# Optimization experiments

Hardware: AMD Instinct MI355X
Metric: run time of the kernel (lower is better)

The kernel has to match this reference:

```python
import jax, jax.numpy as jnp
import numpy as np

D_MODEL = 1024
D_FF = 4096
N_HEADS = 16
HEAD_DIM = D_MODEL // N_HEADS
EPS = 1e-6
B, S = 4, 2048


def _linear_params(key, d_in, d_out):
    kw, kb = jax.random.split(key)
    scale = 1.0 / np.sqrt(d_in)
    w = jax.random.uniform(kw, (d_in, d_out), minval=-scale, maxval=scale, dtype=jnp.float32)
    b = jax.random.uniform(kb, (d_out,), minval=-scale, maxval=scale, dtype=jnp.float32)
    return w, b


def setup_inputs() -> dict:
    key = jax.random.key(0)
    ks = jax.random.split(key, 16)
    x = jax.random.normal(ks[0], (B, S, D_MODEL), dtype=jnp.float32)
    enc = jax.random.normal(ks[1], (B, S, D_MODEL), dtype=jnp.float32)
    # masked self-attention params
    wq1, bq1 = _linear_params(ks[2], D_MODEL, D_MODEL)
    wk1, bk1 = _linear_params(ks[3], D_MODEL, D_MODEL)
    wv1, bv1 = _linear_params(ks[4], D_MODEL, D_MODEL)
    wo1, bo1 = _linear_params(ks[5], D_MODEL, D_MODEL)
    # cross-attention params
    wq2, bq2 = _linear_params(ks[6], D_MODEL, D_MODEL)
    wk2, bk2 = _linear_params(ks[7], D_MODEL, D_MODEL)
    wv2, bv2 = _linear_params(ks[8], D_MODEL, D_MODEL)
    wo2, bo2 = _linear_params(ks[9], D_MODEL, D_MODEL)
    # feed-forward params
    wf1, bf1 = _linear_params(ks[10], D_MODEL, D_FF)
    wf2, bf2 = _linear_params(ks[11], D_FF, D_MODEL)
    # layer norms
    g1 = jnp.ones((D_MODEL,), jnp.float32); be1 = jnp.zeros((D_MODEL,), jnp.float32)
    g2 = jnp.ones((D_MODEL,), jnp.float32); be2 = jnp.zeros((D_MODEL,), jnp.float32)
    g3 = jnp.ones((D_MODEL,), jnp.float32); be3 = jnp.zeros((D_MODEL,), jnp.float32)
    return dict(x=x, encoder_output=enc,
                wq1=wq1, bq1=bq1, wk1=wk1, bk1=bk1, wv1=wv1, bv1=bv1, wo1=wo1, bo1=bo1,
                wq2=wq2, bq2=bq2, wk2=wk2, bk2=bk2, wv2=wv2, bv2=bv2, wo2=wo2, bo2=bo2,
                wf1=wf1, bf1=bf1, wf2=wf2, bf2=bf2,
                g1=g1, be1=be1, g2=g2, be2=be2, g3=g3, be3=be3)


def _layer_norm(x, g, b):
    mu = jnp.mean(x, axis=-1, keepdims=True)
    var = jnp.mean(jnp.square(x - mu), axis=-1, keepdims=True)
    return (x - mu) * jax.lax.rsqrt(var + EPS) * g + b


def _mha(q_in, k_in, v_in, wq, bq, wk, bk, wv, bv, wo, bo, causal):
    b, s, _ = q_in.shape
    q = (q_in @ wq + bq).reshape(b, s, N_HEADS, HEAD_DIM)
    k = (k_in @ wk + bk).reshape(b, -1, N_HEADS, HEAD_DIM)
    v = (v_in @ wv + bv).reshape(b, -1, N_HEADS, HEAD_DIM)
    scores = jnp.einsum('bqhd,bkhd->bhqk', q, k) / np.sqrt(HEAD_DIM)
    if causal:
        mask = jnp.tril(jnp.ones((s, s), dtype=bool))
        scores = jnp.where(mask, scores, jnp.finfo(scores.dtype).min)
    attn = jax.nn.softmax(scores, axis=-1)
    out = jnp.einsum('bhqk,bkhd->bqhd', attn, v).reshape(b, s, D_MODEL)
    return out @ wo + bo


def reference(x, encoder_output,
              wq1, bq1, wk1, bk1, wv1, bv1, wo1, bo1,
              wq2, bq2, wk2, bk2, wv2, bv2, wo2, bo2,
              wf1, bf1, wf2, bf2,
              g1, be1, g2, be2, g3, be3):
    # masked self-attention + residual + LN
    residual = x
    x = _mha(x, x, x, wq1, bq1, wk1, bk1, wv1, bv1, wo1, bo1, causal=True)
    x = _layer_norm(x + residual, g1, be1)
    # cross-attention (note: q=enc, k=enc, v=x as in the original) + residual + LN
    residual = x
    x = _mha(encoder_output, encoder_output, x, wq2, bq2, wk2, bk2, wv2, bv2, wo2, bo2, causal=False)
    x = _layer_norm(x + residual, g2, be2)
    # feed-forward (dropout=0 -> identity in eval) + residual + LN
    residual = x
    x = jax.nn.relu(x @ wf1 + bf1) @ wf2 + bf2
    x = _layer_norm(x + residual, g3, be3)
    return x
```

## Files before the change

kernel.cpp:

```cpp
#include <hip/hip_runtime.h>


typedef _Float16 f16;
typedef _Float16 f16x8 __attribute__((ext_vector_type(8)));
typedef _Float16 f16x4 __attribute__((ext_vector_type(4)));
typedef __fp16 fp16x2 __attribute__((ext_vector_type(2)));
typedef float f32x4 __attribute__((ext_vector_type(4)));
typedef float f32x16 __attribute__((ext_vector_type(16)));
typedef unsigned int u32;

#define AS1 __attribute__((address_space(1)))
#define AS3 __attribute__((address_space(3)))

constexpr int S_LEN = 2048;
constexpr int DM    = 1024;

constexpr long OFF_W   = 0;
constexpr long OFF_XB  = 32L  << 20;
constexpr long OFF_ENC = 48L  << 20;
constexpr long OFF_Q   = 64L  << 20;
constexpr long OFF_K   = 80L  << 20;
constexpr long OFF_V   = 96L  << 20;
constexpr long OFF_VT  = 112L << 20;
constexpr long OFF_AC  = 128L << 20;
constexpr long OFF_HID = 144L << 20;
constexpr long OFF_F1  = 208L << 20;
constexpr long OFF_F2  = 240L << 20;
constexpr long OFF_F3  = 272L << 20;
constexpr long BUF_BYTES = 304L << 20;

__device__ alignas(4096) unsigned char g_buf[BUF_BYTES];

constexpr long WQ1T = OFF_W + (0L  << 20);
constexpr long WF1T = OFF_W + (16L << 20);
constexpr long WF2T = OFF_W + (24L << 20);
constexpr long WO1T = OFF_W + (6L  << 20);
constexpr long WQ2T = OFF_W + (8L  << 20);
constexpr long WV2T = OFF_W + (12L << 20);
constexpr long WO2T = OFF_W + (14L << 20);

__global__ __launch_bounds__(256) void cvt2_k(const float* __restrict__ x,
                                              const float* __restrict__ enc)
{
    const int bid = blockIdx.x;
    const bool second = bid >= 8192;
    const float* in = second ? enc : x;
    f16* out = (f16*)(g_buf + (second ? OFF_ENC : OFF_XB));
    long i = (long)(second ? bid - 8192 : bid) * 256 + threadIdx.x;
    float4 v = ((const float4*)in)[i];
    f16x4 h;
    h.x = (f16)v.x; h.y = (f16)v.y; h.z = (f16)v.z; h.w = (f16)v.w;
    *(f16x4*)(out + i * 4) = h;
}

struct TWJobs { const float* src[10]; };

__global__ __launch_bounds__(256) void transw_all_k(TWJobs jobs)
{
    __shared__ float t[32][33];
    const int bid = blockIdx.x;
    int j, local;
    if (bid < 8192)       { j = bid >> 10; local = bid & 1023; }
    else if (bid < 12288) { j = 8; local = bid - 8192; }
    else                  { j = 9; local = bid - 12288; }
    const int K = (j == 9) ? 4096 : 1024;
    const int N = (j == 8) ? 4096 : 1024;
    const int tnx = N >> 5;
    const int tx32 = local % tnx, ty32 = local / tnx;
    const long dstOff = (j < 8) ? (long)j * (2L << 20) : ((j == 8) ? WF1T : WF2T);
    const float* W = jobs.src[j];
    f16* Wt = (f16*)(g_buf + dstOff);

    int tx = threadIdx.x, ty = threadIdx.y;
    int c0 = tx32 * 32, r0 = ty32 * 32;
#pragma unroll
    for (int i = 0; i < 4; ++i)
        t[ty + 8*i][tx] = W[(long)(r0 + ty + 8*i) * N + c0 + tx];
    __syncthreads();
#pragma unroll
    for (int i = 0; i < 4; ++i)
        Wt[(long)(c0 + ty + 8*i) * K + r0 + tx] = (f16)t[tx][ty + 8*i];
}

template<int MODE>
__global__ __launch_bounds__(256) void gemm3_k(
    long aOff, long bOff, long cOff, long vtOff,
    const float* __restrict__ b0, const float* __restrict__ b1,
    const float* __restrict__ b2, const float* __restrict__ b3,
    int K, int lda, int ldb, int ldc, long chunkStride, int tvch)
{
    __shared__ alignas(16) f16 As[3][128 * 32];
    __shared__ alignas(16) f16 Bs[3][128 * 32];

    const int tid  = threadIdx.x;
    const int lane = tid & 63;
    const int w    = tid >> 6;
    const int cB   = lane & 15;
    const int hi   = lane >> 4;

    const int nwg = gridDim.x * gridDim.y;
    const int id  = blockIdx.y * gridDim.x + blockIdx.x;
    const int swz = (id & 7) * (nwg >> 3) + (id >> 3);
    const int bx  = swz % gridDim.x, by = swz / gridDim.x;
    const int row0 = by * 128, col0 = bx * 128;

    const f16* Ab = (const f16*)(g_buf + aOff);
    const f16* Bb = (const f16*)(g_buf + bOff);

    const int wr = (w >> 1) * 64;
    const int wc = (w & 1) * 64;

    f32x4 acc[4][4] = {};

    auto stage = [&](int buf, int kt) {
        const int kB = kt * 32;
        const int base = w * 64;
#pragma unroll
        for (int r = 0; r < 2; ++r) {
            const int idx  = r * 256 + base + lane;
            const int srow = idx >> 2, sb = idx & 3;
            const int gk = (sb ^ ((srow >> 1) & 3)) << 3;
            __builtin_amdgcn_global_load_lds(
                (const AS1 void*)(Ab + (long)(row0 + srow) * lda + kB + gk),
                (AS3 void*)(&As[buf][(r * 256 + base) * 8]), 16, 0, 0);
            __builtin_amdgcn_global_load_lds(
                (const AS1 void*)(Bb + (long)(col0 + srow) * ldb + kB + gk),
                (AS3 void*)(&Bs[buf][(r * 256 + base) * 8]), 16, 0, 0);
        }
    };

    const int nt = K >> 5;
    stage(0, 0);
    stage(1, 1);

    for (int t = 0; t < nt; ++t) {
        if (nt - t >= 2) asm volatile("s_waitcnt vmcnt(4)" ::: "memory");
        else             asm volatile("s_waitcnt vmcnt(0)" ::: "memory");
        __builtin_amdgcn_s_barrier();
        __builtin_amdgcn_sched_barrier(0);
        if (t + 2 < nt) stage((t + 2) % 3, t + 2);

        const int cur = t % 3;
        f16x8 af[4], bf[4];
#pragma unroll
        for (int m = 0; m < 4; ++m) {
            const int row = wr + m * 16 + cB;
            af[m] = *(const f16x8*)&As[cur][row * 32 + ((hi ^ ((row >> 1) & 3)) << 3)];
        }
#pragma unroll
        for (int n = 0; n < 4; ++n) {
            const int row = wc + n * 16 + cB;
            bf[n] = *(const f16x8*)&Bs[cur][row * 32 + ((hi ^ ((row >> 1) & 3)) << 3)];
        }
#pragma unroll
        for (int m = 0; m < 4; ++m)
#pragma unroll
            for (int n = 0; n < 4; ++n)
                acc[m][n] = __builtin_amdgcn_mfma_f32_16x16x32_f16(af[m], bf[n], acc[m][n], 0, 0, 0);
    }

    const int ch = col0 >> 10;
    const float* bp = (ch == 0) ? b0 : (ch == 1) ? b1 : (ch == 2) ? b2 : b3;

    if (MODE == 0 && ch == tvch) {
        f16* Vt = (f16*)(g_buf + vtOff);
#pragma unroll
        for (int m = 0; m < 4; ++m) {
#pragma unroll
            for (int n = 0; n < 4; ++n) {
                const int c = col0 + wc + n * 16 + cB;
                const int hh = (c >> 6) & 15, dd = c & 63;
                const float bv = bp[c & 1023];
                const int r0e = row0 + wr + m * 16 + hi * 4;
                const int bb = r0e >> 11, sS = r0e & 2047;
                f16x4 hv;
#pragma unroll
                for (int jj = 0; jj < 4; ++jj) hv[jj] = (f16)(acc[m][n][jj] + bv);
                *(f16x4*)(Vt + (((long)(bb * 16 + hh) * 64 + dd) * 2048 + sS)) = hv;
            }
        }
        return;
    }

    float* Cf = (float*)(g_buf + cOff);
    f16*  Ch = (f16*)(g_buf + cOff);
    const long cBase = (long)ch * chunkStride;
#pragma unroll
    for (int m = 0; m < 4; ++m) {
#pragma unroll
        for (int n = 0; n < 4; ++n) {
            const int c = col0 + wc + n * 16 + cB;
            const float bv = bp[c & 1023];
#pragma unroll
            for (int jj = 0; jj < 4; ++jj) {
                const int r = row0 + wr + m * 16 + hi * 4 + jj;
                float v = acc[m][n][jj] + bv;
                if constexpr (MODE == 1) v = fmaxf(v, 0.f);
                const long idx = cBase + (long)r * ldc + (c & 1023);
                if constexpr (MODE == 2) Cf[idx] = v;
                else                     Ch[idx] = (f16)v;
            }
        }
    }
}

template<int CAUSAL>
__global__ __launch_bounds__(256, 4) void flash_k(long qOff, long kOff, long vtOff, long oOff)
{
    __shared__ alignas(16) f16 KV[2][2][4096];

    const int tid  = threadIdx.x;
    const int lane = tid & 63;
    const int w    = tid >> 6;
    const int ql   = lane & 31;
    const int s    = lane >> 5;

    const int raw   = (int)blockIdx.y * (int)gridDim.x + (int)blockIdx.x;
    const int newid = (raw & 7) * 128 + (raw >> 3);
    const int bh    = newid >> 4;
    int qt = newid & 15;
    if (CAUSAL) qt = 15 - qt;

    const int b = bh >> 4, h = bh & 15;
    const int q0 = qt * 128;
    const long tokB = (long)b * S_LEN;

    const f16* Qb  = (const f16*)(g_buf + qOff);
    const f16* Kb  = (const f16*)(g_buf + kOff);
    const f16* Vtb = (const f16*)(g_buf + vtOff) + (long)bh * 64 * S_LEN;
    f16* Ob = (f16*)(g_buf + oOff);

    const int r8 = lane >> 3;
    const int c8 = lane & 7;
    const int sb = c8 ^ r8;
    const int nch = CAUSAL ? 2 * (qt + 1) : (S_LEN / 64);

    auto stage = [&](int buf, int c) {
        const int kv0s = c * 64;
#pragma unroll
        for (int t = 0; t < 2; ++t) {
            const int grp = w * 2 + t;
            const int row = grp * 8 + r8;
            __builtin_amdgcn_global_load_lds(
                (const AS1 void*)(Kb + (tokB + kv0s + row) * DM + h * 64 + sb * 8),
                (AS3 void*)(&KV[buf][0][grp * 512]), 16, 0, 0);
            __builtin_amdgcn_global_load_lds(
                (const AS1 void*)(Vtb + (long)row * S_LEN + kv0s + sb * 8),
                (AS3 void*)(&KV[buf][1][grp * 512]), 16, 0, 0);
        }
    };

    stage(0, 0);

    f16x8 qf[4];
    {
        const f16 hs = (f16)(0.125f * 1.44269504088896f);
        const f16* qrow = Qb + (tokB + q0 + w * 32 + ql) * DM + h * 64 + s * 8;
#pragma unroll
        for (int kk = 0; kk < 4; ++kk) {
            qf[kk] = *(const f16x8*)(qrow + kk * 16);
#pragma unroll
            for (int i = 0; i < 8; ++i) qf[kk][i] = qf[kk][i] * hs;
        }
    }

    f32x16 oacc[2] = {};
    float mrow = -1e30f, lrow = 0.f;

    for (int c = 0; c < nch; ++c) {
        const int cur = c & 1;
        const int kv0 = c * 64;

        asm volatile("s_waitcnt vmcnt(0) lgkmcnt(0)" ::: "memory");
        __builtin_amdgcn_sched_barrier(0);
        __builtin_amdgcn_s_barrier();
        __builtin_amdgcn_sched_barrier(0);
        if (c + 1 < nch) stage(cur ^ 1, c + 1);

        const bool active = !CAUSAL || (kv0 <= q0 + w * 32 + 31);
        if (active) {
            f32x16 p[2] = {};
#pragma unroll
            for (int kk = 0; kk < 4; ++kk) {
                const int t16 = (kk * 2 + s) ^ (ql & 7);
                f16x8 kf0 = *(const f16x8*)((const char*)&KV[cur][0][0] + ql * 128 + t16 * 16);
                f16x8 kf1 = *(const f16x8*)((const char*)&KV[cur][0][0] + (32 + ql) * 128 + t16 * 16);
                p[0] = __builtin_amdgcn_mfma_f32_32x32x16_f16(kf0, qf[kk], p[0], 0, 0, 0);
                p[1] = __builtin_amdgcn_mfma_f32_32x32x16_f16(kf1, qf[kk], p[1], 0, 0, 0);
            }

            if (CAUSAL && (kv0 + 63 > q0 + w * 32)) {
                const int q = q0 + w * 32 + ql;
#pragma unroll
                for (int v = 0; v < 2; ++v)
#pragma unroll
                    for (int r = 0; r < 16; ++r) {
                        const int kv = kv0 + v * 32 + (r & 3) + 8 * (r >> 2) + 4 * s;
                        if (kv > q) p[v][r] = -1e30f;
                    }
            }

            float rmax = fmaxf(p[0][0], p[0][1]);
#pragma unroll
            for (int r = 2; r < 16; r += 2) rmax = fmaxf(fmaxf(p[0][r], p[0][r + 1]), rmax);
#pragma unroll
            for (int r = 0; r < 16; r += 2) rmax = fmaxf(fmaxf(p[1][r], p[1][r + 1]), rmax);
            rmax = fmaxf(rmax, __shfl_xor(rmax, 32));

            if (!__all(rmax <= mrow + 8.0f)) {
                const float mn = fmaxf(mrow, rmax);
                const float alpha = __builtin_amdgcn_exp2f(mrow - mn);
                lrow *= alpha;
                mrow = mn;
#pragma unroll
                for (int r = 0; r < 16; ++r) {
                    const int qr = (r & 3) + 8 * (r >> 2) + 4 * s;
                    const float ab = __shfl(alpha, qr);
                    oacc[0][r] *= ab;
                    oacc[1][r] *= ab;
                }
            }

            u32 pk[2][4][2];
            float rsum = 0.f;
#pragma unroll
            for (int v = 0; v < 2; ++v)
#pragma unroll
                for (int a = 0; a < 4; ++a)
#pragma unroll
                    for (int cc = 0; cc < 2; ++cc) {
                        const float e0 = __builtin_amdgcn_exp2f(p[v][4 * a + 2 * cc] - mrow);
                        const float e1 = __builtin_amdgcn_exp2f(p[v][4 * a + 2 * cc + 1] - mrow);
                        rsum += e0 + e1;
                        union { fp16x2 h; u32 u; } cv;
                        cv.h = __builtin_amdgcn_cvt_pkrtz(e0, e1);
                        pk[v][a][cc] = cv.u;
                    }
            rsum += __shfl_xor(rsum, 32);
            lrow += rsum;

            u32 loc[2][2][2], exv[2][2][2];
#pragma unroll
            for (int v = 0; v < 2; ++v)
#pragma unroll
                for (int k1 = 0; k1 < 2; ++k1)
#pragma unroll
                    for (int cc = 0; cc < 2; ++cc) {
                        const u32 pe = pk[v][2 * k1][cc];
                        const u32 po = pk[v][2 * k1 + 1][cc];
                        loc[v][k1][cc] = s ? po : pe;
                        const u32 snd = s ? pe : po;
                        exv[v][k1][cc] = (u32)__shfl_xor((int)snd, 32);
                    }

#pragma unroll
            for (int ks = 0; ks < 4; ++ks) {
                const int v = ks >> 1, k1 = ks & 1;
                union { u32 u[4]; f16x8 hv; } pa;
                pa.u[0] = s ? exv[v][k1][0] : loc[v][k1][0];
                pa.u[1] = s ? exv[v][k1][1] : loc[v][k1][1];
                pa.u[2] = s ? loc[v][k1][0] : exv[v][k1][0];
                pa.u[3] = s ? loc[v][k1][1] : exv[v][k1][1];
                const int tv = (ks * 2 + s) ^ (ql & 7);
                f16x8 vf0 = *(const f16x8*)((const char*)&KV[cur][1][0] + ql * 128 + tv * 16);
                f16x8 vf1 = *(const f16x8*)((const char*)&KV[cur][1][0] + (32 + ql) * 128 + tv * 16);
                oacc[0] = __builtin_amdgcn_mfma_f32_32x32x16_f16(pa.hv, vf0, oacc[0], 0, 0, 0);
                oacc[1] = __builtin_amdgcn_mfma_f32_32x32x16_f16(pa.hv, vf1, oacc[1], 0, 0, 0);
            }
        }
    }

    asm volatile("s_waitcnt lgkmcnt(0)" ::: "memory");
    __builtin_amdgcn_sched_barrier(0);
    __builtin_amdgcn_s_barrier();

    f16* Es = ((f16*)&KV[0][0][0]) + w * 2304;
    const float linv = 1.0f / lrow;
#pragma unroll
    for (int r = 0; r < 16; ++r) {
        const int qr = (r & 3) + 8 * (r >> 2) + 4 * s;
        const float lb = __shfl(linv, qr);
        Es[qr * 72 + ql]      = (f16)(oacc[0][r] * lb);
        Es[qr * 72 + 32 + ql] = (f16)(oacc[1][r] * lb);
    }
    const int orow = lane >> 1;
    const int oh   = (lane & 1) * 32;
    const f16* srcp = ((const f16*)&KV[0][0][0]) + w * 2304 + orow * 72 + oh;
    f16* dst = Ob + (tokB + q0 + w * 32 + orow) * DM + h * 64 + oh;
#pragma unroll
    for (int t = 0; t < 4; ++t)
        *(f16x8*)(dst + t * 8) = *(const f16x8*)(srcp + t * 8);
}

__global__ __launch_bounds__(256) void ln_k(
    long inOff, const float* __restrict__ residExt, long residOff,
    const float* __restrict__ gamma, const float* __restrict__ beta,
    float* __restrict__ outFExt, long outFOff, long outHOff)
{
    const float* in    = (const float*)(g_buf + inOff);
    const float* resid = residExt ? residExt : (const float*)(g_buf + residOff);
    float* outF = outFExt ? outFExt : (float*)(g_buf + outFOff);
    f16*  outH = (f16*)(g_buf + outHOff);

    const long row = blockIdx.x;
    const int tid = threadIdx.x;
    const int lane = tid & 63, wid = tid >> 6;

    float4 a  = ((const float4*)(in    + row * DM))[tid];
    float4 rr = ((const float4*)(resid + row * DM))[tid];
    float x0 = a.x + rr.x, x1 = a.y + rr.y, x2 = a.z + rr.z, x3 = a.w + rr.w;

    __shared__ float red[4];
    float ss = x0 + x1 + x2 + x3;
#pragma unroll
    for (int o = 32; o > 0; o >>= 1) ss += __shfl_xor(ss, o);
    if (lane == 0) red[wid] = ss;
    __syncthreads();
    const float mu = (red[0] + red[1] + red[2] + red[3]) * (1.0f / DM);

    float d0 = x0 - mu, d1 = x1 - mu, d2 = x2 - mu, d3 = x3 - mu;
    float qq = d0*d0 + d1*d1 + d2*d2 + d3*d3;
#pragma unroll
    for (int o = 32; o > 0; o >>= 1) qq += __shfl_xor(qq, o);
    __syncthreads();
    if (lane == 0) red[wid] = qq;
    __syncthreads();
    const float var = (red[0] + red[1] + red[2] + red[3]) * (1.0f / DM);
    const float rs = rsqrtf(var + 1e-6f);

    float4 g  = ((const float4*)gamma)[tid];
    float4 be = ((const float4*)beta)[tid];
    float y0 = d0 * rs * g.x + be.x;
    float y1 = d1 * rs * g.y + be.y;
    float y2 = d2 * rs * g.z + be.z;
    float y3 = d3 * rs * g.w + be.w;

    ((float4*)(outF + row * DM))[tid] = make_float4(y0, y1, y2, y3);
    f16x4 hh; hh.x = (f16)y0; hh.y = (f16)y1; hh.z = (f16)y2; hh.w = (f16)y3;
    *(f16x4*)(outH + row * DM + tid * 4) = hh;
}

extern "C" void kernel_launch(void* const* d_in, const int* in_sizes, int n_in,
                              void* d_out, int out_size, void* d_ws, size_t ws_size,
                              hipStream_t stream)
{
    (void)in_sizes; (void)n_in; (void)d_ws; (void)ws_size; (void)out_size;
    const float* x   = (const float*)d_in[0];
    const float* enc = (const float*)d_in[1];
    const float* wq1 = (const float*)d_in[2];  const float* bq1 = (const float*)d_in[3];
    const float* wk1 = (const float*)d_in[4];  const float* bk1 = (const float*)d_in[5];
    const float* wv1 = (const float*)d_in[6];  const float* bv1 = (const float*)d_in[7];
    const float* wo1 = (const float*)d_in[8];  const float* bo1 = (const float*)d_in[9];
    const float* wq2 = (const float*)d_in[10]; const float* bq2 = (const float*)d_in[11];
    const float* wk2 = (const float*)d_in[12]; const float* bk2 = (const float*)d_in[13];
    const float* wv2 = (const float*)d_in[14]; const float* bv2 = (const float*)d_in[15];
    const float* wo2 = (const float*)d_in[16]; const float* bo2 = (const float*)d_in[17];
    const float* wf1 = (const float*)d_in[18]; const float* bf1 = (const float*)d_in[19];
    const float* wf2 = (const float*)d_in[20]; const float* bf2 = (const float*)d_in[21];
    const float* g1  = (const float*)d_in[22]; const float* be1 = (const float*)d_in[23];
    const float* g2  = (const float*)d_in[24]; const float* be2 = (const float*)d_in[25];
    const float* g3  = (const float*)d_in[26]; const float* be3 = (const float*)d_in[27];
    float* out = (float*)d_out;

    const dim3 T256(256), T32x8(32, 8);
    const long QKV_CHUNK = 8192L * 1024;

    cvt2_k<<<16384, T256, 0, stream>>>(x, enc);
    TWJobs jobs;
    jobs.src[0] = wq1; jobs.src[1] = wk1; jobs.src[2] = wv1; jobs.src[3] = wo1;
    jobs.src[4] = wq2; jobs.src[5] = wk2; jobs.src[6] = wv2; jobs.src[7] = wo2;
    jobs.src[8] = wf1; jobs.src[9] = wf2;
    transw_all_k<<<16384, T32x8, 0, stream>>>(jobs);

    gemm3_k<0><<<dim3(24, 64), T256, 0, stream>>>(OFF_XB, WQ1T, OFF_Q, OFF_VT,
        bq1, bk1, bv1, bv1, 1024, 1024, 1024, 1024, QKV_CHUNK, 2);
    flash_k<1><<<dim3(16, 64), T256, 0, stream>>>(OFF_Q, OFF_K, OFF_VT, OFF_AC);
    gemm3_k<2><<<dim3(8, 64), T256, 0, stream>>>(OFF_AC, WO1T, OFF_F2, 0,
        bo1, bo1, bo1, bo1, 1024, 1024, 1024, 1024, 1024, -1);
    ln_k<<<8192, T256, 0, stream>>>(OFF_F2, x, 0, g1, be1, nullptr, OFF_F1, OFF_XB);

    gemm3_k<0><<<dim3(16, 64), T256, 0, stream>>>(OFF_ENC, WQ2T, OFF_Q, 0,
        bq2, bk2, bk2, bk2, 1024, 1024, 1024, 1024, QKV_CHUNK, -1);
    gemm3_k<0><<<dim3(8, 64), T256, 0, stream>>>(OFF_XB, WV2T, OFF_V, OFF_VT,
        bv2, bv2, bv2, bv2, 1024, 1024, 1024, 1024, 1024, 0);
    flash_k<0><<<dim3(16, 64), T256, 0, stream>>>(OFF_Q, OFF_K, OFF_VT, OFF_AC);
    gemm3_k<2><<<dim3(8, 64), T256, 0, stream>>>(OFF_AC, WO2T, OFF_F2, 0,
        bo2, bo2, bo2, bo2, 1024, 1024, 1024, 1024, 1024, -1);
    ln_k<<<8192, T256, 0, stream>>>(OFF_F2, nullptr, OFF_F1, g2, be2, nullptr, OFF_F3, OFF_XB);

    gemm3_k<1><<<dim3(32, 64), T256, 0, stream>>>(OFF_XB, WF1T, OFF_HID, 0,
        bf1, bf1 + 1024, bf1 + 2048, bf1 + 3072, 1024, 1024, 1024, 4096, 1024, -1);
    gemm3_k<2><<<dim3(8, 64), T256, 0, stream>>>(OFF_HID, WF2T, OFF_F2, 0,
        bf2, bf2, bf2, bf2, 4096, 4096, 4096, 1024, 1024, -1);
    ln_k<<<8192, T256, 0, stream>>>(OFF_F2, nullptr, OFF_F3, g3, be3, out, 0, OFF_XB);
}
```

Before: 693.0 us.

## Split-K the N=1024 output GEMMs and raise MFMA wave priority

The three fp32-output GEMMs (attention output projections and FFN down-projection) that launched only 512 workgroups now use a two-way split-K over a z grid dimension. The second half writes an unbiased partial into a new scratch buffer, which the following layer-norm kernel adds in. This is meant to fill more compute units on 256-CU hardware, at the cost of an extra fp32 partial write and read. Separately, s_setprio is raised around the MFMA blocks in both the GEMM and flash-attention kernels to favour matrix-issuing waves.

```diff
diff --git a/kernel.cpp b/kernel.cpp
--- a/kernel.cpp
+++ b/kernel.cpp
@@ -15,19 +15,20 @@
 constexpr int S_LEN = 2048;
 constexpr int DM    = 1024;
 
-constexpr long OFF_W   = 0;
-constexpr long OFF_XB  = 32L  << 20;
-constexpr long OFF_ENC = 48L  << 20;
-constexpr long OFF_Q   = 64L  << 20;
-constexpr long OFF_K   = 80L  << 20;
-constexpr long OFF_V   = 96L  << 20;
-constexpr long OFF_VT  = 112L << 20;
-constexpr long OFF_AC  = 128L << 20;
-constexpr long OFF_HID = 144L << 20;
-constexpr long OFF_F1  = 208L << 20;
-constexpr long OFF_F2  = 240L << 20;
-constexpr long OFF_F3  = 272L << 20;
-constexpr long BUF_BYTES = 304L << 20;
+constexpr long OFF_W    = 0;
+constexpr long OFF_XB   = 32L  << 20;
+constexpr long OFF_ENC  = 48L  << 20;
+constexpr long OFF_Q    = 64L  << 20;
+constexpr long OFF_K    = 80L  << 20;
+constexpr long OFF_V    = 96L  << 20;
+constexpr long OFF_VT   = 112L << 20;
+constexpr long OFF_AC   = 128L << 20;
+constexpr long OFF_HID  = 144L << 20;
+constexpr long OFF_F1   = 208L << 20;
+constexpr long OFF_F2   = 240L << 20;
+constexpr long OFF_F3   = 272L << 20;
+constexpr long OFF_PART = 304L << 20;
+constexpr long BUF_BYTES = 336L << 20;
 
 __device__ alignas(4096) unsigned char g_buf[BUF_BYTES];
 
@@ -84,7 +85,7 @@
 
 template<int MODE>
 __global__ __launch_bounds__(256) void gemm3_k(
-    long aOff, long bOff, long cOff, long vtOff,
+    long aOff, long bOff, long cOff, long partOff, long vtOff,
     const float* __restrict__ b0, const float* __restrict__ b1,
     const float* __restrict__ b2, const float* __restrict__ b3,
     int K, int lda, int ldb, int ldc, long chunkStride, int tvch)
@@ -98,14 +99,18 @@
     const int cB   = lane & 15;
     const int hi   = lane >> 4;
 
-    const int nwg = gridDim.x * gridDim.y;
-    const int id  = blockIdx.y * gridDim.x + blockIdx.x;
+    const int gx = gridDim.x, gy = gridDim.y;
+    const int nwg = gx * gy * gridDim.z;
+    const int id  = ((int)blockIdx.z * gy + (int)blockIdx.y) * gx + (int)blockIdx.x;
     const int swz = (id & 7) * (nwg >> 3) + (id >> 3);
-    const int bx  = swz % gridDim.x, by = swz / gridDim.x;
+    const int bx  = swz % gx;
+    const int rem = swz / gx;
+    const int by  = rem % gy;
+    const int bz  = rem / gy;
     const int row0 = by * 128, col0 = bx * 128;
 
-    const f16* Ab = (const f16*)(g_buf + aOff);
-    const f16* Bb = (const f16*)(g_buf + bOff);
+    const f16* Ab = (const f16*)(g_buf + aOff) + (long)bz * K;
+    const f16* Bb = (const f16*)(g_buf + bOff) + (long)bz * K;
 
     const int wr = (w >> 1) * 64;
     const int wc = (w & 1) * 64;
@@ -152,11 +157,13 @@
             const int row = wc + n * 16 + cB;
             bf[n] = *(const f16x8*)&Bs[cur][row * 32 + ((hi ^ ((row >> 1) & 3)) << 3)];
         }
+        __builtin_amdgcn_s_setprio(1);
 #pragma unroll
         for (int m = 0; m < 4; ++m)
 #pragma unroll
             for (int n = 0; n < 4; ++n)
                 acc[m][n] = __builtin_amdgcn_mfma_f32_16x16x32_f16(af[m], bf[n], acc[m][n], 0, 0, 0);
+        __builtin_amdgcn_s_setprio(0);
     }
 
     const int ch = col0 >> 10;
@@ -182,7 +189,7 @@
         return;
     }
 
-    float* Cf = (float*)(g_buf + cOff);
+    float* Cf = (float*)(g_buf + (bz ? partOff : cOff));
     f16*  Ch = (f16*)(g_buf + cOff);
     const long cBase = (long)ch * chunkStride;
 #pragma unroll
@@ -190,7 +197,7 @@
 #pragma unroll
         for (int n = 0; n < 4; ++n) {
             const int c = col0 + wc + n * 16 + cB;
-            const float bv = bp[c & 1023];
+            const float bv = bz ? 0.f : bp[c & 1023];
 #pragma unroll
             for (int jj = 0; jj < 4; ++jj) {
                 const int r = row0 + wr + m * 16 + hi * 4 + jj;
@@ -280,6 +287,7 @@
         const bool active = !CAUSAL || (kv0 <= q0 + w * 32 + 31);
         if (active) {
             f32x16 p[2] = {};
+            __builtin_amdgcn_s_setprio(1);
 #pragma unroll
             for (int kk = 0; kk < 4; ++kk) {
                 const int t16 = (kk * 2 + s) ^ (ql & 7);
@@ -288,6 +296,7 @@
                 p[0] = __builtin_amdgcn_mfma_f32_32x32x16_f16(kf0, qf[kk], p[0], 0, 0, 0);
                 p[1] = __builtin_amdgcn_mfma_f32_32x32x16_f16(kf1, qf[kk], p[1], 0, 0, 0);
             }
+            __builtin_amdgcn_s_setprio(0);
 
             if (CAUSAL && (kv0 + 63 > q0 + w * 32)) {
                 const int q = q0 + w * 32 + ql;
@@ -353,6 +362,7 @@
                         exv[v][k1][cc] = (u32)__shfl_xor((int)snd, 32);
                     }
 
+            __builtin_amdgcn_s_setprio(1);
 #pragma unroll
             for (int ks = 0; ks < 4; ++ks) {
                 const int v = ks >> 1, k1 = ks & 1;
@@ -367,6 +377,7 @@
                 oacc[0] = __builtin_amdgcn_mfma_f32_32x32x16_f16(pa.hv, vf0, oacc[0], 0, 0, 0);
                 oacc[1] = __builtin_amdgcn_mfma_f32_32x32x16_f16(pa.hv, vf1, oacc[1], 0, 0, 0);
             }
+            __builtin_amdgcn_s_setprio(0);
         }
     }
 
@@ -393,7 +404,7 @@
 }
 
 __global__ __launch_bounds__(256) void ln_k(
-    long inOff, const float* __restrict__ residExt, long residOff,
+    long inOff, long in2Off, const float* __restrict__ residExt, long residOff,
     const float* __restrict__ gamma, const float* __restrict__ beta,
     float* __restrict__ outFExt, long outFOff, long outHOff)
 {
@@ -409,6 +420,11 @@
     float4 a  = ((const float4*)(in    + row * DM))[tid];
     float4 rr = ((const float4*)(resid + row * DM))[tid];
     float x0 = a.x + rr.x, x1 = a.y + rr.y, x2 = a.z + rr.z, x3 = a.w + rr.w;
+    if (in2Off >= 0) {
+        const float* in2 = (const float*)(g_buf + in2Off);
+        float4 p = ((const float4*)(in2 + row * DM))[tid];
+        x0 += p.x; x1 += p.y; x2 += p.z; x3 += p.w;
+    }
 
     __shared__ float red[4];
     float ss = x0 + x1 + x2 + x3;
@@ -472,25 +488,25 @@
     jobs.src[8] = wf1; jobs.src[9] = wf2;
     transw_all_k<<<16384, T32x8, 0, stream>>>(jobs);
 
-    gemm3_k<0><<<dim3(24, 64), T256, 0, stream>>>(OFF_XB, WQ1T, OFF_Q, OFF_VT,
+    gemm3_k<0><<<dim3(24, 64, 1), T256, 0, stream>>>(OFF_XB, WQ1T, OFF_Q, 0, OFF_VT,
         bq1, bk1, bv1, bv1, 1024, 1024, 1024, 1024, QKV_CHUNK, 2);
     flash_k<1><<<dim3(16, 64), T256, 0, stream>>>(OFF_Q, OFF_K, OFF_VT, OFF_AC);
-    gemm3_k<2><<<dim3(8, 64), T256, 0, stream>>>(OFF_AC, WO1T, OFF_F2, 0,
-        bo1, bo1, bo1, bo1, 1024, 1024, 1024, 1024, 1024, -1);
-    ln_k<<<8192, T256, 0, stream>>>(OFF_F2, x, 0, g1, be1, nullptr, OFF_F1, OFF_XB);
-
-    gemm3_k<0><<<dim3(16, 64), T256, 0, stream>>>(OFF_ENC, WQ2T, OFF_Q, 0,
+    gemm3_k<2><<<dim3(8, 64, 2), T256, 0, stream>>>(OFF_AC, WO1T, OFF_F2, OFF_PART, 0,
+        bo1, bo1, bo1, bo1, 512, 1024, 1024, 1024, 1024, -1);
+    ln_k<<<8192, T256, 0, stream>>>(OFF_F2, OFF_PART, x, 0, g1, be1, nullptr, OFF_F1, OFF_XB);
+
+    gemm3_k<0><<<dim3(16, 64, 1), T256, 0, stream>>>(OFF_ENC, WQ2T, OFF_Q, 0, 0,
         bq2, bk2, bk2, bk2, 1024, 1024, 1024, 1024, QKV_CHUNK, -1);
-    gemm3_k<0><<<dim3(8, 64), T256, 0, stream>>>(OFF_XB, WV2T, OFF_V, OFF_VT,
+    gemm3_k<0><<<dim3(8, 64, 1), T256, 0, stream>>>(OFF_XB, WV2T, OFF_V, 0, OFF_VT,
         bv2, bv2, bv2, bv2, 1024, 1024, 1024, 1024, 1024, 0);
     flash_k<0><<<dim3(16, 64), T256, 0, stream>>>(OFF_Q, OFF_K, OFF_VT, OFF_AC);
-    gemm3_k<2><<<dim3(8, 64), T256, 0, stream>>>(OFF_AC, WO2T, OFF_F2, 0,
-        bo2, bo2, bo2, bo2, 1024, 1024, 1024, 1024, 1024, -1);
-    ln_k<<<8192, T256, 0, stream>>>(OFF_F2, nullptr, OFF_F1, g2, be2, nullptr, OFF_F3, OFF_XB);
-
-    gemm3_k<1><<<dim3(32, 64), T256, 0, stream>>>(OFF_XB, WF1T, OFF_HID, 0,
+    gemm3_k<2><<<dim3(8, 64, 2), T256, 0, stream>>>(OFF_AC, WO2T, OFF_F2, OFF_PART, 0,
+        bo2, bo2, bo2, bo2, 512, 1024, 1024, 1024, 1024, -1);
+    ln_k<<<8192, T256, 0, stream>>>(OFF_F2, OFF_PART, nullptr, OFF_F1, g2, be2, nullptr, OFF_F3, OFF_XB);
+
+    gemm3_k<1><<<dim3(32, 64, 1), T256, 0, stream>>>(OFF_XB, WF1T, OFF_HID, 0, 0,
         bf1, bf1 + 1024, bf1 + 2048, bf1 + 3072, 1024, 1024, 1024, 4096, 1024, -1);
-    gemm3_k<2><<<dim3(8, 64), T256, 0, stream>>>(OFF_HID, WF2T, OFF_F2, 0,
-        bf2, bf2, bf2, bf2, 4096, 4096, 4096, 1024, 1024, -1);
-    ln_k<<<8192, T256, 0, stream>>>(OFF_F2, nullptr, OFF_F3, g3, be3, out, 0, OFF_XB);
+    gemm3_k<2><<<dim3(8, 64, 2), T256, 0, stream>>>(OFF_HID, WF2T, OFF_F2, OFF_PART, 0,
+        bf2, bf2, bf2, bf2, 2048, 4096, 4096, 1024, 1024, -1);
+    ln_k<<<8192, T256, 0, stream>>>(OFF_F2, OFF_PART, nullptr, OFF_F3, g3, be3, out, 0, OFF_XB);
 }
```

New measurement: 744.3 us. 7.4% more time.
